# Performance work log

Hardware: AMD Instinct MI355X
Metric: run time of the kernel (lower is better)

Reference implementation:

```python
import jax, jax.numpy as jnp
import numpy as np

SCALE = 0.1    # BinarizeConv2dSDP scale factor
BN_EPS = 1e-5

def _binarize(x):
    # straight-through sign binarization (STE): forward = sign(x), grad = identity
    return x + jax.lax.stop_gradient(jnp.sign(x) - x)

def _bin_conv3x3(x, w, stride=1):
    # binarize activations and weights; per-output-channel weight scaling alpha = mean|w|
    a_b = _binarize(x)
    alpha = jnp.mean(jnp.abs(w), axis=(1, 2, 3))          # [Cout]
    w_b = _binarize(w)
    y = jax.lax.conv_general_dilated(
        a_b, w_b, window_strides=(stride, stride), padding=((1, 1), (1, 1)),
        dimension_numbers=('NCHW', 'OIHW', 'NCHW'))
    return y * (SCALE * alpha)[None, :, None, None]

def _batchnorm(x, gamma, beta):
    mu = jnp.mean(x, axis=(0, 2, 3), keepdims=True)
    var = jnp.var(x, axis=(0, 2, 3), keepdims=True)
    xh = (x - mu) * jax.lax.rsqrt(var + BN_EPS)
    return xh * gamma[None, :, None, None] + beta[None, :, None, None]

def _prelu(x, a):
    return jnp.where(x >= 0, x, a.reshape(()) * x)

def setup_inputs() -> dict:
    key = jax.random.key(0)
    ks = jax.random.split(key, 5)
    B, C, H, W = 64, 256, 28, 28
    return {
        'x': jax.random.normal(ks[0], (B, C, H, W), jnp.float32),
        'conv1_w': jax.random.normal(ks[1], (C, C, 3, 3), jnp.float32) * 0.05,
        'conv2_w': jax.random.normal(ks[2], (C, C, 3, 3), jnp.float32) * 0.05,
        'bn1_gamma': jnp.ones((C,), jnp.float32),
        'bn1_beta': jnp.zeros((C,), jnp.float32),
        'bn2_gamma': jnp.ones((C,), jnp.float32),
        'bn2_beta': jnp.zeros((C,), jnp.float32),
        'prelu1_a': jnp.full((1,), 0.25, jnp.float32),
        'prelu2_a': jnp.full((1,), 0.25, jnp.float32),
    }

def reference(x, conv1_w, conv2_w, bn1_gamma, bn1_beta, bn2_gamma, bn2_beta, prelu1_a, prelu2_a):
    residual = x
    out = _bin_conv3x3(x, conv1_w, stride=1)
    out = _batchnorm(out, bn1_gamma, bn1_beta)
    out = out + residual
    out = _prelu(out, prelu1_a)
    residual = out
    out = _bin_conv3x3(out, conv2_w, stride=1)
    out = _batchnorm(out, bn2_gamma, bn2_beta)
    out = out + residual
    out = _prelu(out, prelu2_a)
    return out
```

## Files before the change

### kernel.cpp

```cpp
#include <hip/hip_runtime.h>
#include <cstdint>

#define NB 64
#define NC 256
#define HW 784
#define NPIX (NB*HW)
#define NELEM ((size_t)NB*NC*HW)

typedef int v4i  __attribute__((ext_vector_type(4)));
typedef int v16i __attribute__((ext_vector_type(16)));

union U16 { signed char b[16]; int4 v; };

__global__ __launch_bounds__(256) void alpha_k(
    const float* __restrict__ w1, const float* __restrict__ w2,
    float* __restrict__ al1, float* __restrict__ al2) {
  int blk = blockIdx.x;
  int conv = blk >> 8, cout = blk & 255;
  const float* w = (conv ? w2 : w1) + (size_t)cout * 2304;
  int t = threadIdx.x;
  float s = 0.0f;
  for (int i = t; i < 2304; i += 256) s += fabsf(w[i]);
  __shared__ float red[256];
  red[t] = s;
  __syncthreads();
  for (int st = 128; st > 0; st >>= 1) {
    if (t < st) red[t] += red[t + st];
    __syncthreads();
  }
  if (t == 0) (conv ? al2 : al1)[cout] = red[0] / 2304.0f;
}

__global__ __launch_bounds__(256) void wfrag_k(
    const float* __restrict__ w1, const float* __restrict__ w2,
    signed char* __restrict__ Wf1, signed char* __restrict__ Wf2) {
  int bi = blockIdx.x;
  int conv = bi / 72, r = bi % 72, tap = r >> 3, cg = r & 7;
  const float* w = conv ? w2 : w1;
  signed char* Wf = conv ? Wf2 : Wf1;
  int t = threadIdx.x;
  for (int e = t; e < 512; e += 256) {
    int c = e >> 6, lane = e & 63;
    int cout = cg * 32 + (lane & 31);
    int cin0 = c * 32 + (lane >> 5) * 16;
    U16 u;
#pragma unroll
    for (int bb = 0; bb < 16; ++bb) {
      float v = w[((size_t)cout * 256 + cin0 + bb) * 9 + tap];
      u.b[bb] = v > 0.f ? 1 : (v < 0.f ? -1 : 0);
    }
    *(int4*)(Wf + ((((size_t)tap * 8 + c) * 8 + cg) * 64 + lane) * 16) = u.v;
  }
}

__global__ __launch_bounds__(256) void pack_x(
    const float* __restrict__ in, signed char* __restrict__ A) {
  __shared__ float tile[256 * 33];
  int t = threadIdx.x;
  int P0 = blockIdx.x * 32;
  int pl = t & 31, c0 = t >> 5;
  int P = P0 + pl;
  int b = P / HW, hw = P - b * HW;
  size_t base = (size_t)b * (NC * HW) + (size_t)c0 * HW + hw;
#pragma unroll
  for (int i = 0; i < 32; ++i)
    tile[(i * 8 + c0) * 33 + pl] = in[base + (size_t)i * 8 * HW];
  __syncthreads();
  int g = t >> 4, pls = t & 15;
#pragma unroll
  for (int ph = 0; ph < 2; ++ph) {
    int pp = ph * 16 + pls;
    U16 u;
#pragma unroll
    for (int bb = 0; bb < 16; ++bb) {
      float v = tile[(g * 16 + bb) * 33 + pp];
      u.b[bb] = v > 0.f ? 1 : (v < 0.f ? -1 : 0);
    }
    *(int4*)(A + (size_t)(P0 + pp) * 256 + g * 16) = u.v;
  }
}

__global__ __launch_bounds__(256, 3) void conv_mfma(
    const signed char* __restrict__ A, const signed char* __restrict__ Wf,
    short* __restrict__ dotb,
    int* __restrict__ pd, int* __restrict__ pq) {
  __shared__ signed char As[192 * 256 + 256];
  int t = threadIdx.x;
  int lane = t & 63, wid = t >> 6;
  int mblk = blockIdx.x >> 1, nblk = blockIdx.x & 1;
  int p0 = mblk * 128;
  int wm = wid & 1, wn = wid >> 1;
  int khalf = lane >> 5;

  {
    const signed char* src = A + (size_t)(p0 - 29) * 256;
#pragma unroll
    for (int i = 0; i < 12; ++i) {
      int off = i * 4096 + t * 16;
      int4 d = *(const int4*)(src + off);
      int r = off >> 8, g = (off >> 4) & 15;
      int gs = g ^ ((r + 3) & 15);
      *(int4*)(As + r * 256 + gs * 16) = d;
    }
    if (t < 16) { int4 z = {0, 0, 0, 0}; *(int4*)(As + 192 * 256 + t * 16) = z; }
  }

  int prow[2], hh[2], ww[2];
#pragma unroll
  for (int i = 0; i < 2; ++i) {
    int p = p0 + wm * 64 + i * 32 + (lane & 31);
    prow[i] = p;
    int hw = p % HW;
    hh[i] = hw / 28;
    ww[i] = hw - hh[i] * 28;
  }
  __syncthreads();

  v16i acc[2][2];
  {
    v16i z = {0};
    acc[0][0] = z; acc[0][1] = z; acc[1][0] = z; acc[1][1] = z;
  }

  int cgbase = nblk * 4 + wn * 2;
  const signed char* wlane = Wf + ((size_t)cgbase * 64 + lane) * 16;

  int rbT[2][2], kkT[2][2];
#pragma unroll
  for (int i = 0; i < 2; ++i) {
    int hp = hh[i] - 1, wp = ww[i] - 1;
    bool val = ((unsigned)hp < 28u) && ((unsigned)wp < 28u);
    int pr = prow[i] - 29;
    rbT[0][i] = val ? (pr - (p0 - 29)) * 256 : 192 * 256;
    kkT[0][i] = val ? ((pr & 15) << 4) : 0;
  }

  v4i ab[2][2], wb[2][2];
#pragma unroll
  for (int i = 0; i < 2; ++i)
    ab[0][i] = *(const v4i*)(As + rbT[0][i] + ((khalf << 4) ^ kkT[0][i]));
  wb[0][0] = *(const v4i*)(wlane);
  wb[0][1] = *(const v4i*)(wlane + 1024);

#pragma unroll
  for (int it = 0; it < 72; ++it) {
    const int cur = it & 1, nxt = cur ^ 1;
    const int tp = it >> 3, c = it & 7;

    if (c == 7 && tp < 8) {
      const int tn = tp + 1;
      const int ky = tn / 3, kx = tn % 3;
      const int dlt = (ky - 1) * 28 + (kx - 1);
#pragma unroll
      for (int i = 0; i < 2; ++i) {
        int hp = hh[i] + ky - 1, wp = ww[i] + kx - 1;
        bool val = ((unsigned)hp < 28u) && ((unsigned)wp < 28u);
        int pr = prow[i] + dlt;
        rbT[tn & 1][i] = val ? (pr - (p0 - 29)) * 256 : 192 * 256;
        kkT[tn & 1][i] = val ? ((pr & 15) << 4) : 0;
      }
    }

    if (it < 71) {
      const int it1 = it + 1;
      const int t1 = it1 >> 3, c1 = it1 & 7;
      const int ts = t1 & 1;
#pragma unroll
      for (int i = 0; i < 2; ++i)
        ab[nxt][i] = *(const v4i*)(
            As + rbT[ts][i] + ((((c1 * 2 + khalf)) << 4) ^ kkT[ts][i]));
      const signed char* wt = wlane + (size_t)it1 * 8192;
      wb[nxt][0] = *(const v4i*)(wt);
      wb[nxt][1] = *(const v4i*)(wt + 1024);
    }
    __builtin_amdgcn_sched_barrier(0);

#pragma unroll
    for (int i = 0; i < 2; ++i) {
      acc[i][0] = __builtin_amdgcn_mfma_i32_32x32x32_i8(ab[cur][i], wb[cur][0],
                                                        acc[i][0], 0, 0, 0);
      acc[i][1] = __builtin_amdgcn_mfma_i32_32x32x32_i8(ab[cur][i], wb[cur][1],
                                                        acc[i][1], 0, 0, 0);
    }
  }

#pragma unroll
  for (int j = 0; j < 2; ++j) {
    int s = 0, sq = 0;
#pragma unroll
    for (int i = 0; i < 2; ++i)
#pragma unroll
      for (int q = 0; q < 16; ++q) {
        int v = acc[i][j][q];
        s += v; sq += v * v;
      }
    s += __shfl_xor(s, 32); sq += __shfl_xor(sq, 32);
    if (lane < 32) {
      int row = mblk * 2 + wm;
      pd[row * 256 + nblk * 128 + wn * 64 + j * 32 + lane] = s;
      pq[row * 256 + nblk * 128 + wn * 64 + j * 32 + lane] = sq;
    }
  }

#pragma unroll
  for (int i = 0; i < 2; ++i) {
    int pr = p0 + wm * 64 + i * 32 + 4 * khalf;
#pragma unroll
    for (int j = 0; j < 2; ++j) {
      int cb = nblk * 128 + wn * 64 + j * 32;
#pragma unroll
      for (int q = 0; q < 16; ++q) {
        int row = pr + (q & 3) + 8 * (q >> 2);
        dotb[(size_t)row * 256 + cb + (lane & 31)] = (short)acc[i][j][q];
      }
    }
  }
}

__global__ __launch_bounds__(256) void bn_finalize(
    const int* __restrict__ pd, const int* __restrict__ pq,
    const float* __restrict__ alpha, const float* __restrict__ gamma,
    const float* __restrict__ beta, float* __restrict__ scale,
    float* __restrict__ shift) {
  int c = blockIdx.x, t = threadIdx.x;
  long long D = 0, D2 = 0;
  for (int r = t; r < 784; r += 256) {
    D  += (long long)pd[r * 256 + c];
    D2 += (long long)pq[r * 256 + c];
  }
  __shared__ long long rd[256], rq[256];
  rd[t] = D; rq[t] = D2;
  __syncthreads();
  for (int st = 128; st > 0; st >>= 1) {
    if (t < st) { rd[t] += rd[t + st]; rq[t] += rq[t + st]; }
    __syncthreads();
  }
  if (t == 0) {
    float sc = 0.1f * alpha[c];
    const float invN = 1.0f / (float)(NB * HW);
    float md  = (float)rd[0] * invN;
    float ex2 = (float)rq[0] * invN;
    float var = sc * sc * (ex2 - md * md);
    float rs = rsqrtf(var + 1e-5f);
    float g = gamma[c];
    scale[c] = rs * g * sc;
    shift[c] = beta[c] - sc * md * rs * g;
  }
}

__global__ __launch_bounds__(256) void bn_mid(
    const short* __restrict__ dot, const float* __restrict__ x,
    const float* __restrict__ scale, const float* __restrict__ shift,
    const float* __restrict__ pa, float* __restrict__ a1,
    signed char* __restrict__ A) {
  __shared__ short rawd[32 * 264];
  __shared__ float tile[256 * 33];
  __shared__ float ssc[256], ssh[256];
  int t = threadIdx.x;
  int P0 = blockIdx.x * 32;
  ssc[t] = scale[t]; ssh[t] = shift[t];
  float ap = pa[0];
#pragma unroll
  for (int i = 0; i < 4; ++i) {
    int idx = i * 256 + t;
    int pl = idx >> 5, g = idx & 31;
    int4 d = *(const int4*)(dot + (size_t)(P0 + pl) * 256 + g * 8);
    *(int4*)(&rawd[pl * 264 + g * 8]) = d;
  }
  __syncthreads();
  int pl = t & 31, c0 = t >> 5;
  int P = P0 + pl;
  int b = P / HW, hw = P - b * HW;
  size_t base = (size_t)b * (NC * HW) + (size_t)c0 * HW + hw;
#pragma unroll
  for (int i = 0; i < 32; ++i) {
    int c = i * 8 + c0;
    size_t addr = base + (size_t)i * 8 * HW;
    float d = (float)rawd[pl * 264 + c];
    float v = fmaf(d, ssc[c], ssh[c]) + x[addr];
    float o = v >= 0.0f ? v : ap * v;
    a1[addr] = o;
    tile[c * 33 + pl] = o;
  }
  __syncthreads();
  int g = t >> 4, pls = t & 15;
#pragma unroll
  for (int ph = 0; ph < 2; ++ph) {
    int pp = ph * 16 + pls;
    U16 u;
#pragma unroll
    for (int bb = 0; bb < 16; ++bb) {
      float v = tile[(g * 16 + bb) * 33 + pp];
      u.b[bb] = v > 0.f ? 1 : (v < 0.f ? -1 : 0);
    }
    *(int4*)(A + (size_t)(P0 + pp) * 256 + g * 16) = u.v;
  }
}

__global__ __launch_bounds__(256) void bn_fin_apply(
    const short* __restrict__ dot, const float* __restrict__ res,
    const float* __restrict__ scale, const float* __restrict__ shift,
    const float* __restrict__ pa, float* __restrict__ out) {
  __shared__ short rawd[32 * 264];
  __shared__ float ssc[256], ssh[256];
  int t = threadIdx.x;
  int P0 = blockIdx.x * 32;
  ssc[t] = scale[t]; ssh[t] = shift[t];
  float ap = pa[0];
#pragma unroll
  for (int i = 0; i < 4; ++i) {
    int idx = i * 256 + t;
    int pl = idx >> 5, g = idx & 31;
    int4 d = *(const int4*)(dot + (size_t)(P0 + pl) * 256 + g * 8);
    *(int4*)(&rawd[pl * 264 + g * 8]) = d;
  }
  __syncthreads();
  int pl = t & 31, c0 = t >> 5;
  int P = P0 + pl;
  int b = P / HW, hw = P - b * HW;
  size_t base = (size_t)b * (NC * HW) + (size_t)c0 * HW + hw;
#pragma unroll
  for (int i = 0; i < 32; ++i) {
    int c = i * 8 + c0;
    size_t addr = base + (size_t)i * 8 * HW;
    float d = (float)rawd[pl * 264 + c];
    float v = fmaf(d, ssc[c], ssh[c]) + res[addr];
    out[addr] = v >= 0.0f ? v : ap * v;
  }
}

extern "C" void kernel_launch(void* const* d_in, const int* in_sizes, int n_in,
                              void* d_out, int out_size, void* d_ws, size_t ws_size,
                              hipStream_t stream) {
  const float* x   = (const float*)d_in[0];
  const float* w1  = (const float*)d_in[1];
  const float* w2  = (const float*)d_in[2];
  const float* g1  = (const float*)d_in[3];
  const float* b1  = (const float*)d_in[4];
  const float* g2  = (const float*)d_in[5];
  const float* b2  = (const float*)d_in[6];
  const float* pa1 = (const float*)d_in[7];
  const float* pa2 = (const float*)d_in[8];
  float* out = (float*)d_out;

  char* ws = (char*)d_ws;
  short*       dotb = (short*)ws;       ws += (size_t)NPIX * 256 * 2;
  signed char* Abuf = (signed char*)ws; ws += (size_t)NPIX * 256;
  signed char* Wf1  = (signed char*)ws; ws += 589824;
  signed char* Wf2  = (signed char*)ws; ws += 589824;
  int* pd1 = (int*)ws; ws += 784 * 256 * 4;
  int* pq1 = (int*)ws; ws += 784 * 256 * 4;
  int* pd2 = (int*)ws; ws += 784 * 256 * 4;
  int* pq2 = (int*)ws; ws += 784 * 256 * 4;
  float* alpha1 = (float*)ws; ws += 1024;
  float* alpha2 = (float*)ws; ws += 1024;
  float* scale1 = (float*)ws; ws += 1024;
  float* shift1 = (float*)ws; ws += 1024;
  float* scale2 = (float*)ws; ws += 1024;
  float* shift2 = (float*)ws; ws += 1024;

  alpha_k<<<512, 256, 0, stream>>>(w1, w2, alpha1, alpha2);
  wfrag_k<<<144, 256, 0, stream>>>(w1, w2, Wf1, Wf2);
  pack_x<<<NPIX / 32, 256, 0, stream>>>(x, Abuf);

  conv_mfma<<<784, 256, 0, stream>>>(Abuf, Wf1, dotb, pd1, pq1);
  bn_finalize<<<256, 256, 0, stream>>>(pd1, pq1, alpha1, g1, b1, scale1, shift1);
  bn_mid<<<NPIX / 32, 256, 0, stream>>>(dotb, x, scale1, shift1, pa1, out, Abuf);

  conv_mfma<<<784, 256, 0, stream>>>(Abuf, Wf2, dotb, pd2, pq2);
  bn_finalize<<<256, 256, 0, stream>>>(pd2, pq2, alpha2, g2, b2, scale2, shift2);
  bn_fin_apply<<<NPIX / 32, 256, 0, stream>>>(dotb, out, scale2, shift2, pa2, out);
}
```

Before: 168.1 us.

## Enlarge conv tile to 256 pixels x 256 channels and stage weights through double-buffered LDS

The binary conv GEMM kernel now gives each 512-thread block 256 pixels and all 256 output channels, instead of 128 pixels by 128 channels. Weight fragments are streamed through a double-buffered LDS region, with one barrier per half-tap, so they are no longer loaded per-lane straight from global memory. This aims to raise activation and weight reuse and cut global weight traffic. In exchange it launches only 196 blocks, fewer than 256 CUs, which leaves some CUs idle, and it adds a per-step barrier and about 145KB of dynamic LDS.

```diff
diff --git a/kernel.cpp b/kernel.cpp
--- a/kernel.cpp
+++ b/kernel.cpp
@@ -6,6 +6,12 @@
 #define HW 784
 #define NPIX (NB*HW)
 #define NELEM ((size_t)NB*NC*HW)
+
+#define MTILE 256
+#define A_BYTES (314*256)
+#define ZERO_OFF A_BYTES
+#define W_OFF (A_BYTES + 256)
+#define LDS_TOTAL (W_OFF + 2*32768)
 
 typedef int v4i  __attribute__((ext_vector_type(4)));
 typedef int v16i __attribute__((ext_vector_type(16)));
@@ -80,29 +86,41 @@
   }
 }
 
-__global__ __launch_bounds__(256, 3) void conv_mfma(
+__global__ __launch_bounds__(512, 2) void conv_mfma(
     const signed char* __restrict__ A, const signed char* __restrict__ Wf,
     short* __restrict__ dotb,
     int* __restrict__ pd, int* __restrict__ pq) {
-  __shared__ signed char As[192 * 256 + 256];
+  extern __shared__ signed char smem[];
+  signed char* As = smem;
+  signed char* Wlds = smem + W_OFF;
+
   int t = threadIdx.x;
   int lane = t & 63, wid = t >> 6;
-  int mblk = blockIdx.x >> 1, nblk = blockIdx.x & 1;
-  int p0 = mblk * 128;
-  int wm = wid & 1, wn = wid >> 1;
+  int mblk = blockIdx.x;
+  int p0 = mblk * MTILE;
+  int wm = wid & 3, wn = wid >> 2;
   int khalf = lane >> 5;
 
   {
     const signed char* src = A + (size_t)(p0 - 29) * 256;
 #pragma unroll
-    for (int i = 0; i < 12; ++i) {
-      int off = i * 4096 + t * 16;
-      int4 d = *(const int4*)(src + off);
-      int r = off >> 8, g = (off >> 4) & 15;
-      int gs = g ^ ((r + 3) & 15);
-      *(int4*)(As + r * 256 + gs * 16) = d;
-    }
-    if (t < 16) { int4 z = {0, 0, 0, 0}; *(int4*)(As + 192 * 256 + t * 16) = z; }
+    for (int i = 0; i < 10; ++i) {
+      int off = i * 8192 + t * 16;
+      if (off < A_BYTES) {
+        int4 d = *(const int4*)(src + off);
+        int r = off >> 8, g = (off >> 4) & 15;
+        int gs = g ^ ((r + 3) & 15);
+        *(int4*)(As + r * 256 + gs * 16) = d;
+      }
+    }
+    if (t < 16) { int4 z = {0, 0, 0, 0}; *(int4*)(As + ZERO_OFF + t * 16) = z; }
+  }
+  {
+#pragma unroll
+    for (int k = 0; k < 4; ++k) {
+      int4 d = *(const int4*)(Wf + k * 8192 + t * 16);
+      *(int4*)(Wlds + k * 8192 + t * 16) = d;
+    }
   }
 
   int prow[2], hh[2], ww[2];
@@ -116,76 +134,74 @@
   }
   __syncthreads();
 
-  v16i acc[2][2];
-  {
-    v16i z = {0};
-    acc[0][0] = z; acc[0][1] = z; acc[1][0] = z; acc[1][1] = z;
-  }
-
-  int cgbase = nblk * 4 + wn * 2;
-  const signed char* wlane = Wf + ((size_t)cgbase * 64 + lane) * 16;
-
-  int rbT[2][2], kkT[2][2];
-#pragma unroll
-  for (int i = 0; i < 2; ++i) {
-    int hp = hh[i] - 1, wp = ww[i] - 1;
-    bool val = ((unsigned)hp < 28u) && ((unsigned)wp < 28u);
-    int pr = prow[i] - 29;
-    rbT[0][i] = val ? (pr - (p0 - 29)) * 256 : 192 * 256;
-    kkT[0][i] = val ? ((pr & 15) << 4) : 0;
-  }
-
-  v4i ab[2][2], wb[2][2];
+  v16i acc[2][4];
 #pragma unroll
   for (int i = 0; i < 2; ++i)
-    ab[0][i] = *(const v4i*)(As + rbT[0][i] + ((khalf << 4) ^ kkT[0][i]));
-  wb[0][0] = *(const v4i*)(wlane);
-  wb[0][1] = *(const v4i*)(wlane + 1024);
-
-#pragma unroll
-  for (int it = 0; it < 72; ++it) {
-    const int cur = it & 1, nxt = cur ^ 1;
-    const int tp = it >> 3, c = it & 7;
-
-    if (c == 7 && tp < 8) {
-      const int tn = tp + 1;
-      const int ky = tn / 3, kx = tn % 3;
+#pragma unroll
+    for (int j = 0; j < 4; ++j) { v16i z = {0}; acc[i][j] = z; }
+
+  int rbT[2], kkT[2];
+
+#pragma unroll
+  for (int ht = 0; ht < 18; ++ht) {
+    const int cur = ht & 1;
+
+    if ((ht & 1) == 0) {
+      const int tap = ht >> 1;
+      const int ky = tap / 3, kx = tap % 3;
       const int dlt = (ky - 1) * 28 + (kx - 1);
 #pragma unroll
       for (int i = 0; i < 2; ++i) {
         int hp = hh[i] + ky - 1, wp = ww[i] + kx - 1;
         bool val = ((unsigned)hp < 28u) && ((unsigned)wp < 28u);
         int pr = prow[i] + dlt;
-        rbT[tn & 1][i] = val ? (pr - (p0 - 29)) * 256 : 192 * 256;
-        kkT[tn & 1][i] = val ? ((pr & 15) << 4) : 0;
+        rbT[i] = val ? (pr - (p0 - 29)) * 256 : ZERO_OFF;
+        kkT[i] = val ? ((pr & 15) << 4) : 0;
       }
     }
 
-    if (it < 71) {
-      const int it1 = it + 1;
-      const int t1 = it1 >> 3, c1 = it1 & 7;
-      const int ts = t1 & 1;
-#pragma unroll
-      for (int i = 0; i < 2; ++i)
-        ab[nxt][i] = *(const v4i*)(
-            As + rbT[ts][i] + ((((c1 * 2 + khalf)) << 4) ^ kkT[ts][i]));
-      const signed char* wt = wlane + (size_t)it1 * 8192;
-      wb[nxt][0] = *(const v4i*)(wt);
-      wb[nxt][1] = *(const v4i*)(wt + 1024);
-    }
-    __builtin_amdgcn_sched_barrier(0);
-
-#pragma unroll
-    for (int i = 0; i < 2; ++i) {
-      acc[i][0] = __builtin_amdgcn_mfma_i32_32x32x32_i8(ab[cur][i], wb[cur][0],
-                                                        acc[i][0], 0, 0, 0);
-      acc[i][1] = __builtin_amdgcn_mfma_i32_32x32x32_i8(ab[cur][i], wb[cur][1],
-                                                        acc[i][1], 0, 0, 0);
-    }
-  }
-
-#pragma unroll
-  for (int j = 0; j < 2; ++j) {
+    int4 wreg0, wreg1, wreg2, wreg3;
+    if (ht < 17) {
+      const signed char* wsrc = Wf + (size_t)(ht + 1) * 32768 + t * 16;
+      wreg0 = *(const int4*)(wsrc);
+      wreg1 = *(const int4*)(wsrc + 8192);
+      wreg2 = *(const int4*)(wsrc + 16384);
+      wreg3 = *(const int4*)(wsrc + 24576);
+    }
+
+#pragma unroll
+    for (int c = 0; c < 4; ++c) {
+      const int gch = (ht & 1) * 4 + c;
+      v4i a0 = *(const v4i*)(As + rbT[0] + (((gch * 2 + khalf) << 4) ^ kkT[0]));
+      v4i a1 = *(const v4i*)(As + rbT[1] + (((gch * 2 + khalf) << 4) ^ kkT[1]));
+      const signed char* wb =
+          Wlds + cur * 32768 + (c * 8 + wn * 4) * 1024 + lane * 16;
+      v4i w0 = *(const v4i*)(wb);
+      v4i w1 = *(const v4i*)(wb + 1024);
+      v4i w2 = *(const v4i*)(wb + 2048);
+      v4i w3 = *(const v4i*)(wb + 3072);
+      acc[0][0] = __builtin_amdgcn_mfma_i32_32x32x32_i8(a0, w0, acc[0][0], 0, 0, 0);
+      acc[0][1] = __builtin_amdgcn_mfma_i32_32x32x32_i8(a0, w1, acc[0][1], 0, 0, 0);
+      acc[0][2] = __builtin_amdgcn_mfma_i32_32x32x32_i8(a0, w2, acc[0][2], 0, 0, 0);
+      acc[0][3] = __builtin_amdgcn_mfma_i32_32x32x32_i8(a0, w3, acc[0][3], 0, 0, 0);
+      acc[1][0] = __builtin_amdgcn_mfma_i32_32x32x32_i8(a1, w0, acc[1][0], 0, 0, 0);
+      acc[1][1] = __builtin_amdgcn_mfma_i32_32x32x32_i8(a1, w1, acc[1][1], 0, 0, 0);
+      acc[1][2] = __builtin_amdgcn_mfma_i32_32x32x32_i8(a1, w2, acc[1][2], 0, 0, 0);
+      acc[1][3] = __builtin_amdgcn_mfma_i32_32x32x32_i8(a1, w3, acc[1][3], 0, 0, 0);
+    }
+
+    if (ht < 17) {
+      signed char* wdst = Wlds + (cur ^ 1) * 32768 + t * 16;
+      *(int4*)(wdst)         = wreg0;
+      *(int4*)(wdst + 8192)  = wreg1;
+      *(int4*)(wdst + 16384) = wreg2;
+      *(int4*)(wdst + 24576) = wreg3;
+      __syncthreads();
+    }
+  }
+
+#pragma unroll
+  for (int j = 0; j < 4; ++j) {
     int s = 0, sq = 0;
 #pragma unroll
     for (int i = 0; i < 2; ++i)
@@ -196,9 +212,10 @@
       }
     s += __shfl_xor(s, 32); sq += __shfl_xor(sq, 32);
     if (lane < 32) {
-      int row = mblk * 2 + wm;
-      pd[row * 256 + nblk * 128 + wn * 64 + j * 32 + lane] = s;
-      pq[row * 256 + nblk * 128 + wn * 64 + j * 32 + lane] = sq;
+      int row = mblk * 4 + wm;
+      int co = wn * 128 + j * 32 + lane;
+      pd[row * 256 + co] = s;
+      pq[row * 256 + co] = sq;
     }
   }
 
@@ -206,8 +223,8 @@
   for (int i = 0; i < 2; ++i) {
     int pr = p0 + wm * 64 + i * 32 + 4 * khalf;
 #pragma unroll
-    for (int j = 0; j < 2; ++j) {
-      int cb = nblk * 128 + wn * 64 + j * 32;
+    for (int j = 0; j < 4; ++j) {
+      int cb = wn * 128 + j * 32;
 #pragma unroll
       for (int q = 0; q < 16; ++q) {
         int row = pr + (q & 3) + 8 * (q >> 2);
@@ -359,15 +376,22 @@
   float* scale2 = (float*)ws; ws += 1024;
   float* shift2 = (float*)ws; ws += 1024;
 
+  static int attr_done = 0;
+  if (!attr_done) {
+    hipFuncSetAttribute((const void*)conv_mfma,
+                        hipFuncAttributeMaxDynamicSharedMemorySize, LDS_TOTAL);
+    attr_done = 1;
+  }
+
   alpha_k<<<512, 256, 0, stream>>>(w1, w2, alpha1, alpha2);
   wfrag_k<<<144, 256, 0, stream>>>(w1, w2, Wf1, Wf2);
   pack_x<<<NPIX / 32, 256, 0, stream>>>(x, Abuf);
 
-  conv_mfma<<<784, 256, 0, stream>>>(Abuf, Wf1, dotb, pd1, pq1);
+  conv_mfma<<<196, 512, LDS_TOTAL, stream>>>(Abuf, Wf1, dotb, pd1, pq1);
   bn_finalize<<<256, 256, 0, stream>>>(pd1, pq1, alpha1, g1, b1, scale1, shift1);
   bn_mid<<<NPIX / 32, 256, 0, stream>>>(dotb, x, scale1, shift1, pa1, out, Abuf);
 
-  conv_mfma<<<784, 256, 0, stream>>>(Abuf, Wf2, dotb, pd2, pq2);
+  conv_mfma<<<196, 512, LDS_TOTAL, stream>>>(Abuf, Wf2, dotb, pd2, pq2);
   bn_finalize<<<256, 256, 0, stream>>>(pd2, pq2, alpha2, g2, b2, scale2, shift2);
   bn_fin_apply<<<NPIX / 32, 256, 0, stream>>>(dotb, out, scale2, shift2, pa2, out);
 }
```

Result: faster. 164.1 us (-2.4%).
